# Kernel tuning notes

Measured on AMD Instinct MI355X. Metric: run time of the kernel, lower is better.

The kernel has to match this reference:

```python
import jax, jax.numpy as jnp
import numpy as np

NEG_SLOPE = 0.2  # PyG GATConv default negative_slope


def gat_layer(x, src, dst, N, W, att_src, att_dst, bias, heads, out_ch, concat):
    # x: [N, Fin]; W: [Fin, heads*out_ch]; att_*: [heads, out_ch]; bias matches output dim
    h = (x @ W).reshape(N, heads, out_ch)              # [N, H, C]
    a_src = (h * att_src).sum(-1)                      # [N, H]
    a_dst = (h * att_dst).sum(-1)                      # [N, H]
    e = jax.nn.leaky_relu(a_src[src] + a_dst[dst], NEG_SLOPE)  # [E, H]
    # segment softmax over incoming edges of each destination node
    e_max = jax.ops.segment_max(e, dst, num_segments=N)        # [N, H]
    e_exp = jnp.exp(e - e_max[dst])                             # [E, H]
    denom = jax.ops.segment_sum(e_exp, dst, num_segments=N)    # [N, H]
    alpha = e_exp / (denom[dst] + 1e-16)                        # [E, H]
    msg = alpha[:, :, None] * h[src]                            # [E, H, C]
    out = jax.ops.segment_sum(msg, dst, num_segments=N)        # [N, H, C]
    out = out.reshape(N, heads * out_ch) if concat else out.mean(axis=1)
    return out + bias


def setup_inputs() -> dict:
    key = jax.random.key(0)
    ks = jax.random.split(key, 10)
    N, E = 40000, 160000
    Fin, H1, C1 = 602, 8, 256
    H2, C2 = 1, 42
    g = lambda k, shape, fan: (jax.random.normal(k, shape, dtype=jnp.float32) * (1.0 / np.sqrt(fan)))
    return {
        "x": jax.random.normal(ks[0], (N, Fin), dtype=jnp.float32),
        "edge_index": jax.random.randint(ks[1], (2, E), 0, N, dtype=jnp.int64),
        "W1": g(ks[2], (Fin, H1 * C1), Fin),
        "att_src1": g(ks[3], (H1, C1), C1),
        "att_dst1": g(ks[4], (H1, C1), C1),
        "b1": jnp.zeros((H1 * C1,), dtype=jnp.float32),
        "W2": g(ks[5], (H1 * C1, H2 * C2), H1 * C1),
        "att_src2": g(ks[6], (H2, C2), C2),
        "att_dst2": g(ks[7], (H2, C2), C2),
        "b2": jnp.zeros((C2,), dtype=jnp.float32),
    }


def reference(x, edge_index, W1, att_src1, att_dst1, b1, W2, att_src2, att_dst2, b2):
    N = x.shape[0]
    # PyG GATConv default add_self_loops=True
    loops = jnp.arange(N, dtype=edge_index.dtype)
    src = jnp.concatenate([edge_index[0], loops])
    dst = jnp.concatenate([edge_index[1], loops])
    h = gat_layer(x, src, dst, N, W1, att_src1, att_dst1, b1, heads=8, out_ch=256, concat=True)
    h = jax.nn.relu(h)  # dropout is identity in eval mode
    h = gat_layer(h, src, dst, N, W2, att_src2, att_dst2, b2, heads=1, out_ch=42, concat=False)
    return jax.nn.log_softmax(h, axis=1)
```

## Files before the change

kernel.cpp:

```cpp
#include <hip/hip_runtime.h>
#include <hip/hip_bf16.h>

#define NN   40000
#define NE   160000
#define ETOT 200000
#define FIN  602
#define NH1  8
#define C1   256
#define F1   2048
#define C2   42
#define NEG  0.2f
#define NB   157
#define KP   608
#define MP   40064

typedef unsigned short u16;
typedef unsigned int   u32;
typedef __bf16 bf16x8 __attribute__((ext_vector_type(8)));
typedef float  f32x4  __attribute__((ext_vector_type(4)));

__device__ __forceinline__ float bfu(u16 v){ return __uint_as_float(((u32)v) << 16); }
__device__ __forceinline__ float bflo(u32 u){ return __uint_as_float(u << 16); }
__device__ __forceinline__ float bfhi(u32 u){ return __uint_as_float(u & 0xffff0000u); }
__device__ __forceinline__ u16 f2bf(float f){
  u32 u = __float_as_uint(f);
  u32 r = (u + 0x7fffu + ((u >> 16) & 1u)) >> 16;
  return (u16)r;
}

__device__ __forceinline__ void gl_lds16(const u16* g, u16* l) {
  __builtin_amdgcn_global_load_lds(
      (const __attribute__((address_space(1))) u32*)(g),
      (__attribute__((address_space(3))) u32*)(l), 16, 0, 0);
}

__global__ void probe_k(const u32* __restrict__ xw, const int* __restrict__ ei,
                        int* __restrict__ flags) {
  if (threadIdx.x == 0) {
    int zc = 0;
    for (int k = 0; k < 64; ++k) zc += (ei[2*k + 1] == 0) ? 1 : 0;
    flags[0] = (zc == 64) ? 1 : 0;
    int inr = 0;
    for (int k = 0; k < 64; ++k) {
      u32 low = xw[k] & 0xffffu;
      int e = (int)((low >> 7) & 0xff);
      inr += (e >= 100 && e <= 140) ? 1 : 0;
    }
    flags[1] = (inr >= 32) ? 0 : 1;
  }
}

__global__ void cvt_f32_k(const void* __restrict__ src, float* __restrict__ dst, int n,
                          const int* __restrict__ flags) {
  int i = blockIdx.x * 256 + threadIdx.x;
  if (i >= n) return;
  dst[i] = flags[1] ? ((const float*)src)[i] : bfu(((const u16*)src)[i]);
}

__global__ void xb_k(const void* __restrict__ x, u16* __restrict__ xb,
                     const int* __restrict__ flags) {
  int k = blockIdx.x * 256 + threadIdx.x;
  int row = blockIdx.y;
  if (k >= KP) return;
  u16 v = 0;
  if (row < NN && k < FIN)
    v = flags[1] ? f2bf(((const float*)x)[(size_t)row * FIN + k])
                 : ((const u16*)x)[(size_t)row * FIN + k];
  xb[(size_t)row * KP + k] = v;
}

__global__ void w1t_k(const void* __restrict__ W1, u16* __restrict__ w1t,
                      const int* __restrict__ flags) {
  int n = blockIdx.x * 256 + threadIdx.x;
  int k = blockIdx.y;
  if (n >= F1) return;
  u16 v = 0;
  if (k < FIN) v = flags[1] ? f2bf(((const float*)W1)[(size_t)k * F1 + n])
                            : ((const u16*)W1)[(size_t)k * F1 + n];
  w1t[(size_t)n * KP + k] = v;
}

__global__ void w2t_k(const void* __restrict__ W2, u16* __restrict__ w2t,
                      const int* __restrict__ flags) {
  int i = blockIdx.x * 256 + threadIdx.x;
  if (i >= 64 * F1) return;
  int c = i >> 11, k = i & (F1 - 1);
  u16 v = 0;
  if (c < C2) v = flags[1] ? f2bf(((const float*)W2)[(size_t)k * C2 + c])
                           : ((const u16*)W2)[(size_t)k * C2 + c];
  w2t[i] = v;
}

__device__ __forceinline__ void edge_sd(const int* __restrict__ ei, int e, int imode,
                                        int& s, int& d) {
  if (e < NE) {
    if (imode) { s = ei[2*e]; d = ei[2*(NE + e)]; }
    else       { s = ei[e];   d = ei[NE + e];     }
  } else { s = d = e - NE; }
}

__global__ void deg_k(const int* __restrict__ ei, int* __restrict__ deg,
                      const int* __restrict__ flags) {
  int e = blockIdx.x * 256 + threadIdx.x;
  if (e >= ETOT) return;
  int s, d; edge_sd(ei, e, flags[0], s, d);
  atomicAdd(&deg[d], 1);
}

__global__ __launch_bounds__(256) void scan1_k(const int* __restrict__ deg,
                                               int* __restrict__ tmp, int* __restrict__ bsum) {
  __shared__ int s[256];
  int b = blockIdx.x, t = threadIdx.x, i = b * 256 + t;
  int v = (i < NN) ? deg[i] : 0;
  s[t] = v; __syncthreads();
  for (int o = 1; o < 256; o <<= 1) {
    int u = (t >= o) ? s[t - o] : 0;
    __syncthreads(); s[t] += u; __syncthreads();
  }
  if (i < NN) tmp[i] = s[t];
  if (t == 255) bsum[b] = s[255];
}

__global__ __launch_bounds__(256) void scan2_k(int* __restrict__ bsum) {
  __shared__ int s[256];
  int t = threadIdx.x;
  int v = (t < NB) ? bsum[t] : 0;
  s[t] = v; __syncthreads();
  for (int o = 1; o < 256; o <<= 1) {
    int u = (t >= o) ? s[t - o] : 0;
    __syncthreads(); s[t] += u; __syncthreads();
  }
  if (t < NB) bsum[t] = s[t];
}

__global__ void scan3_k(const int* __restrict__ deg, const int* __restrict__ tmp,
                        const int* __restrict__ bsum, int* __restrict__ start, int* __restrict__ cur) {
  int i = blockIdx.x * 256 + threadIdx.x;
  if (i >= NN) return;
  int b = i >> 8;
  int off = b ? bsum[b - 1] : 0;
  int excl = tmp[i] - deg[i] + off;
  start[i] = excl; cur[i] = excl;
}

__global__ void fill_k(const int* __restrict__ ei, int* __restrict__ cur,
                       int* __restrict__ csr_src, int* __restrict__ csr_dst,
                       const int* __restrict__ flags) {
  int e = blockIdx.x * 256 + threadIdx.x;
  if (e >= ETOT) return;
  int s, d; edge_sd(ei, e, flags[0], s, d);
  int pos = atomicAdd(&cur[d], 1);
  csr_src[pos] = s; csr_dst[pos] = d;
}

__global__ __launch_bounds__(256) void gemm1a_k(const u16* __restrict__ xb,
                                                const u16* __restrict__ w1t,
                                                u16* __restrict__ h1,
                                                const float* __restrict__ as1c,
                                                const float* __restrict__ ad1c,
                                                float* __restrict__ a_s1,
                                                float* __restrict__ a_d1) {
  __shared__ u16 As[128 * 32];
  __shared__ u16 Bs[128 * 32];
  const int t = threadIdx.x;
  const int lane = t & 63, wid = t >> 6;
  const int wr = wid >> 1, wc = wid & 1;
  const int m0 = blockIdx.y * 128, n0 = blockIdx.x * 128;
  const int l16 = lane & 15, lk = (lane >> 4) * 8;
  f32x4 acc[4][4];
  #pragma unroll
  for (int i = 0; i < 4; ++i)
    #pragma unroll
    for (int j = 0; j < 4; ++j) acc[i][j] = (f32x4){0.f, 0.f, 0.f, 0.f};

  const size_t sa0 = (size_t)(m0 + (t >> 2)) * KP + (t & 3) * 8;
  const size_t sa1 = (size_t)(m0 + 64 + (t >> 2)) * KP + (t & 3) * 8;
  const size_t sb0 = (size_t)(n0 + (t >> 2)) * KP + (t & 3) * 8;
  const size_t sb1 = (size_t)(n0 + 64 + (t >> 2)) * KP + (t & 3) * 8;
  u16* la0 = As + (wid << 9);
  u16* la1 = As + 2048 + (wid << 9);
  u16* lb0 = Bs + (wid << 9);
  u16* lb1 = Bs + 2048 + (wid << 9);

  for (int k0 = 0; k0 < KP; k0 += 32) {
    gl_lds16(xb + sa0 + k0, la0);
    gl_lds16(xb + sa1 + k0, la1);
    gl_lds16(w1t + sb0 + k0, lb0);
    gl_lds16(w1t + sb1 + k0, lb1);
    __syncthreads();
    bf16x8 bfr[4];
    #pragma unroll
    for (int ni = 0; ni < 4; ++ni)
      bfr[ni] = *(const bf16x8*)&Bs[(wc * 64 + ni * 16 + l16) * 32 + lk];
    #pragma unroll
    for (int mi = 0; mi < 4; ++mi) {
      bf16x8 af = *(const bf16x8*)&As[(wr * 64 + mi * 16 + l16) * 32 + lk];
      #pragma unroll
      for (int ni = 0; ni < 4; ++ni)
        acc[mi][ni] = __builtin_amdgcn_mfma_f32_16x16x32_bf16(af, bfr[ni], acc[mi][ni], 0, 0, 0);
    }
    __syncthreads();
  }

  const int h0 = n0 >> 8;
  float psrc[4][4], pdst[4][4];
  #pragma unroll
  for (int mi = 0; mi < 4; ++mi)
    #pragma unroll
    for (int r = 0; r < 4; ++r) { psrc[mi][r] = 0.f; pdst[mi][r] = 0.f; }
  #pragma unroll
  for (int ni = 0; ni < 4; ++ni) {
    int col = n0 + wc * 64 + ni * 16 + l16;
    float wsv = as1c[col], wdv = ad1c[col];
    #pragma unroll
    for (int mi = 0; mi < 4; ++mi)
      #pragma unroll
      for (int r = 0; r < 4; ++r) {
        float v = acc[mi][ni][r];
        psrc[mi][r] += v * wsv;
        pdst[mi][r] += v * wdv;
      }
  }
  #pragma unroll
  for (int o = 1; o < 16; o <<= 1) {
    #pragma unroll
    for (int mi = 0; mi < 4; ++mi)
      #pragma unroll
      for (int r = 0; r < 4; ++r) {
        psrc[mi][r] += __shfl_xor(psrc[mi][r], o, 64);
        pdst[mi][r] += __shfl_xor(pdst[mi][r], o, 64);
      }
  }
  const int lr4 = (lane >> 4) * 4;
  if (l16 == 0) {
    #pragma unroll
    for (int mi = 0; mi < 4; ++mi)
      #pragma unroll
      for (int r = 0; r < 4; ++r) {
        int row = m0 + wr * 64 + mi * 16 + lr4 + r;
        if (row < NN) {
          atomicAdd(&a_s1[row * NH1 + h0], psrc[mi][r]);
          atomicAdd(&a_d1[row * NH1 + h0], pdst[mi][r]);
        }
      }
  }

  #pragma unroll
  for (int mi = 0; mi < 4; ++mi) {
    #pragma unroll
    for (int r = 0; r < 4; ++r) {
      int row = m0 + wr * 64 + mi * 16 + lr4 + r;
      if (row < NN) {
        #pragma unroll
        for (int ni = 0; ni < 4; ++ni) {
          int col = n0 + wc * 64 + ni * 16 + l16;
          h1[(size_t)row * F1 + col] = f2bf(acc[mi][ni][r]);
        }
      }
    }
  }
}

__global__ __launch_bounds__(256) void gemm1m_k(const void* __restrict__ xv,
                                                const u16* __restrict__ w1t,
                                                u16* __restrict__ h1,
                                                const int* __restrict__ flags) {
  __shared__ u16 As[128][40];
  __shared__ u16 Bs[128][40];
  const int fm = flags[1];
  const int t = threadIdx.x;
  const int lane = t & 63, wid = t >> 6;
  const int wr = wid >> 1, wc = wid & 1;
  const int m0 = blockIdx.y * 128, n0 = blockIdx.x * 128;
  const int l16 = lane & 15, lk = (lane >> 4) * 8;
  f32x4 acc[4][4];
  #pragma unroll
  for (int i = 0; i < 4; ++i)
    #pragma unroll
    for (int j = 0; j < 4; ++j) acc[i][j] = (f32x4){0.f, 0.f, 0.f, 0.f};
  const int arow = t >> 2;
  const int akb  = (t & 3) * 8;
  for (int k0 = 0; k0 < KP; k0 += 32) {
    #pragma unroll
    for (int i = 0; i < 2; ++i) {
      int row = arow + i * 64;
      int rg = m0 + row;
      u32 d0 = 0, d1 = 0, d2 = 0, d3 = 0;
      if (rg < NN) {
        if (k0 + 32 <= FIN) {
          if (fm) {
            const float* xp = (const float*)xv + (size_t)rg * FIN + k0 + akb;
            float2 p0 = *(const float2*)(xp);
            float2 p1 = *(const float2*)(xp + 2);
            float2 p2 = *(const float2*)(xp + 4);
            float2 p3 = *(const float2*)(xp + 6);
            d0 = (u32)f2bf(p0.x) | ((u32)f2bf(p0.y) << 16);
            d1 = (u32)f2bf(p1.x) | ((u32)f2bf(p1.y) << 16);
            d2 = (u32)f2bf(p2.x) | ((u32)f2bf(p2.y) << 16);
            d3 = (u32)f2bf(p3.x) | ((u32)f2bf(p3.y) << 16);
          } else {
            const u16* xp = (const u16*)xv + (size_t)rg * FIN + k0 + akb;
            d0 = *(const u32*)(xp);
            d1 = *(const u32*)(xp + 2);
            d2 = *(const u32*)(xp + 4);
            d3 = *(const u32*)(xp + 6);
          }
        } else {
          u16 e[8];
          #pragma unroll
          for (int q = 0; q < 8; ++q) {
            int k = k0 + akb + q;
            e[q] = 0;
            if (k < FIN)
              e[q] = fm ? f2bf(((const float*)xv)[(size_t)rg * FIN + k])
                        : ((const u16*)xv)[(size_t)rg * FIN + k];
          }
          d0 = (u32)e[0] | ((u32)e[1] << 16);
          d1 = (u32)e[2] | ((u32)e[3] << 16);
          d2 = (u32)e[4] | ((u32)e[5] << 16);
          d3 = (u32)e[6] | ((u32)e[7] << 16);
        }
      }
      *(uint4*)&As[row][akb] = make_uint4(d0, d1, d2, d3);
      const u16* wp = w1t + (size_t)(n0 + row) * KP + k0 + akb;
      *(uint4*)&Bs[row][akb] = *(const uint4*)wp;
    }
    __syncthreads();
    bf16x8 bfr[4];
    #pragma unroll
    for (int ni = 0; ni < 4; ++ni)
      bfr[ni] = *(const bf16x8*)&Bs[wc * 64 + ni * 16 + l16][lk];
    #pragma unroll
    for (int mi = 0; mi < 4; ++mi) {
      bf16x8 af = *(const bf16x8*)&As[wr * 64 + mi * 16 + l16][lk];
      #pragma unroll
      for (int ni = 0; ni < 4; ++ni)
        acc[mi][ni] = __builtin_amdgcn_mfma_f32_16x16x32_bf16(af, bfr[ni], acc[mi][ni], 0, 0, 0);
    }
    __syncthreads();
  }
  const int lr4 = (lane >> 4) * 4;
  #pragma unroll
  for (int mi = 0; mi < 4; ++mi) {
    #pragma unroll
    for (int r = 0; r < 4; ++r) {
      int row = m0 + wr * 64 + mi * 16 + lr4 + r;
      if (row < NN) {
        #pragma unroll
        for (int ni = 0; ni < 4; ++ni) {
          int col = n0 + wc * 64 + ni * 16 + l16;
          h1[(size_t)row * F1 + col] = f2bf(acc[mi][ni][r]);
        }
      }
    }
  }
}

__global__ __launch_bounds__(256) void att1_k(const u16* __restrict__ h1,
                                              const float* __restrict__ as1c, const float* __restrict__ ad1c,
                                              float* __restrict__ a_s, float* __restrict__ a_d) {
  int n = blockIdx.x, t = threadIdx.x;
  int h = t >> 5, l = t & 31;
  int base = h * C1 + l * 8;
  const u16* hp = h1 + (size_t)n * F1 + base;
  uint4 v = *(const uint4*)hp;
  u32 w[4] = {v.x, v.y, v.z, v.w};
  float ss = 0.f, sd = 0.f;
  #pragma unroll
  for (int p = 0; p < 4; ++p) {
    float e0 = bflo(w[p]), e1 = bfhi(w[p]);
    ss += e0 * as1c[base + 2*p] + e1 * as1c[base + 2*p + 1];
    sd += e0 * ad1c[base + 2*p] + e1 * ad1c[base + 2*p + 1];
  }
  #pragma unroll
  for (int o = 16; o > 0; o >>= 1) {
    ss += __shfl_down(ss, o, 32);
    sd += __shfl_down(sd, o, 32);
  }
  if (l == 0) { a_s[n * NH1 + h] = ss; a_d[n * NH1 + h] = sd; }
}

__global__ __launch_bounds__(256) void gfuse_k(const int* __restrict__ start, const int* __restrict__ deg,
                                               const int* __restrict__ csr_src,
                                               const float* __restrict__ a_s1, const float* __restrict__ a_d1,
                                               const u16* __restrict__ h1, const float* __restrict__ b1c,
                                               const u16* __restrict__ w2t, float* __restrict__ h2) {
  __shared__ u16 rowsL[16 * F1];
  int t = threadIdx.x;
  int nb = blockIdx.x * 16;
  int h = t >> 5;
  int c0 = t * 8;
  float4 bA = *(const float4*)(b1c + c0);
  float4 bB = *(const float4*)(b1c + c0 + 4);
  for (int i = 0; i < 16; ++i) {
    int n = nb + i;
    int s0 = start[n], jend = s0 + deg[n];
    float ad = a_d1[n * NH1 + h];
    float a0=0.f,a1=0.f,a2=0.f,a3=0.f,a4=0.f,a5=0.f,a6=0.f,a7=0.f,den=0.f;
    int j = s0;
    for (; j + 2 <= jend; j += 2) {
      int sA = csr_src[j], sB = csr_src[j + 1];
      float vA = a_s1[sA * NH1 + h] + ad;
      float vB = a_s1[sB * NH1 + h] + ad;
      vA = vA > 0.f ? vA : NEG * vA;
      vB = vB > 0.f ? vB : NEG * vB;
      float eA = expf(vA), eB = expf(vB);
      uint4 uA = *(const uint4*)(h1 + (size_t)sA * F1 + c0);
      uint4 uB = *(const uint4*)(h1 + (size_t)sB * F1 + c0);
      den += eA + eB;
      a0 += eA * bflo(uA.x) + eB * bflo(uB.x);
      a1 += eA * bfhi(uA.x) + eB * bfhi(uB.x);
      a2 += eA * bflo(uA.y) + eB * bflo(uB.y);
      a3 += eA * bfhi(uA.y) + eB * bfhi(uB.y);
      a4 += eA * bflo(uA.z) + eB * bflo(uB.z);
      a5 += eA * bfhi(uA.z) + eB * bfhi(uB.z);
      a6 += eA * bflo(uA.w) + eB * bflo(uB.w);
      a7 += eA * bfhi(uA.w) + eB * bfhi(uB.w);
    }
    if (j < jend) {
      int sA = csr_src[j];
      float vA = a_s1[sA * NH1 + h] + ad;
      vA = vA > 0.f ? vA : NEG * vA;
      float eA = expf(vA);
      uint4 uA = *(const uint4*)(h1 + (size_t)sA * F1 + c0);
      den += eA;
      a0 += eA * bflo(uA.x); a1 += eA * bfhi(uA.x);
      a2 += eA * bflo(uA.y); a3 += eA * bfhi(uA.y);
      a4 += eA * bflo(uA.z); a5 += eA * bfhi(uA.z);
      a6 += eA * bflo(uA.w); a7 += eA * bfhi(uA.w);
    }
    float inv = 1.f / (den + 1e-16f);
    u16 o0 = f2bf(fmaxf(a0 * inv + bA.x, 0.f));
    u16 o1 = f2bf(fmaxf(a1 * inv + bA.y, 0.f));
    u16 o2 = f2bf(fmaxf(a2 * inv + bA.z, 0.f));
    u16 o3 = f2bf(fmaxf(a3 * inv + bA.w, 0.f));
    u16 o4 = f2bf(fmaxf(a4 * inv + bB.x, 0.f));
    u16 o5 = f2bf(fmaxf(a5 * inv + bB.y, 0.f));
    u16 o6 = f2bf(fmaxf(a6 * inv + bB.z, 0.f));
    u16 o7 = f2bf(fmaxf(a7 * inv + bB.w, 0.f));
    uint4 pk;
    pk.x = (u32)o0 | ((u32)o1 << 16);
    pk.y = (u32)o2 | ((u32)o3 << 16);
    pk.z = (u32)o4 | ((u32)o5 << 16);
    pk.w = (u32)o6 | ((u32)o7 << 16);
    int sw = (i & 7) << 3;
    *(uint4*)&rowsL[i * F1 + (c0 ^ sw)] = pk;
  }
  __syncthreads();
  int lane = t & 63, wid = t >> 6;
  int l16 = lane & 15, lk = (lane >> 4) * 8;
  const u16* wt = w2t + (size_t)(wid * 16 + l16) * F1;
  int sw = (l16 & 7) << 3;
  f32x4 acc2 = (f32x4){0.f, 0.f, 0.f, 0.f};
  for (int k0 = 0; k0 < F1; k0 += 32) {
    int kk = k0 + lk;
    bf16x8 af = *(const bf16x8*)&rowsL[l16 * F1 + (kk ^ sw)];
    bf16x8 bf = *(const bf16x8*)(wt + kk);
    acc2 = __builtin_amdgcn_mfma_f32_16x16x32_bf16(af, bf, acc2, 0, 0, 0);
  }
  int col = wid * 16 + l16;
  if (col < C2) {
    int mb = (lane >> 4) * 4;
    #pragma unroll
    for (int r = 0; r < 4; ++r)
      h2[(size_t)(nb + mb + r) * C2 + col] = acc2[r];
  }
}

__global__ __launch_bounds__(64) void att2_k(const float* __restrict__ h2,
                                             const float* __restrict__ as2, const float* __restrict__ ad2,
                                             float* __restrict__ a_s, float* __restrict__ a_d) {
  int n = blockIdx.x, t = threadIdx.x;
  float ss = 0.f, sd = 0.f;
  if (t < C2) {
    float v = h2[(size_t)n * C2 + t];
    ss = v * as2[t];
    sd = v * ad2[t];
  }
  #pragma unroll
  for (int o = 32; o > 0; o >>= 1) {
    ss += __shfl_down(ss, o, 64);
    sd += __shfl_down(sd, o, 64);
  }
  if (t == 0) { a_s[n] = ss; a_d[n] = sd; }
}

__global__ __launch_bounds__(64) void gath2_k(const int* __restrict__ start, const int* __restrict__ deg,
                                              const int* __restrict__ csr_src,
                                              const float* __restrict__ a_s, const float* __restrict__ a_d,
                                              const float* __restrict__ h2, const float* __restrict__ b2,
                                              void* __restrict__ outv, const int* __restrict__ flags) {
  int n = blockIdx.x, t = threadIdx.x;
  int s0 = start[n], cnt = deg[n];
  float ad = a_d[n];
  float acc = 0.f, den = 0.f;
  for (int j = s0; j < s0 + cnt; ++j) {
    int s = csr_src[j];
    float v = a_s[s] + ad;
    v = v > 0.f ? v : NEG * v;
    float e = expf(v);
    den += e;
    if (t < C2) acc += e * h2[(size_t)s * C2 + t];
  }
  float raw = (t < C2) ? acc / (den + 1e-16f) + b2[t] : -1e30f;
  float m = raw;
  #pragma unroll
  for (int o = 32; o > 0; o >>= 1) m = fmaxf(m, __shfl_down(m, o, 64));
  m = __shfl(m, 0, 64);
  float e2 = (t < C2) ? expf(raw - m) : 0.f;
  float ssum = e2;
  #pragma unroll
  for (int o = 32; o > 0; o >>= 1) ssum += __shfl_down(ssum, o, 64);
  ssum = __shfl(ssum, 0, 64);
  if (t < C2) {
    float v = raw - m - logf(ssum);
    if (flags[1]) ((float*)outv)[(size_t)n * C2 + t] = v;
    else          ((u16*) outv)[(size_t)n * C2 + t] = f2bf(v);
  }
}

extern "C" void kernel_launch(void* const* d_in, const int* in_sizes, int n_in,
                              void* d_out, int out_size, void* d_ws, size_t ws_size,
                              hipStream_t stream) {
  const void* x   = d_in[0];
  const int*  ei  = (const int*)d_in[1];
  const void* W1  = d_in[2];
  const void* as1 = d_in[3];
  const void* ad1 = d_in[4];
  const void* b1  = d_in[5];
  const void* W2  = d_in[6];
  const void* as2 = d_in[7];
  const void* ad2 = d_in[8];
  const void* b2  = d_in[9];

  char* ws = (char*)d_ws;
  u16*   h1      = (u16*)  (ws);
  float* ex1     = (float*)(ws + 163840000);
  float* h2      = (float*)(ws + 170240000);
  float* a_s1    = (float*)(ws + 176960000);
  float* a_d1    = (float*)(ws + 178240000);
  float* a_s2    = (float*)(ws + 179520000);
  float* a_d2    = (float*)(ws + 179680000);
  int*   deg     = (int*)  (ws + 179840000);
  int*   start   = (int*)  (ws + 180000000);
  int*   cur     = (int*)  (ws + 180160000);
  int*   tmp     = (int*)  (ws + 180320000);
  int*   csr_src = (int*)  (ws + 180480000);
  int*   csr_dst = (int*)  (ws + 181280000);
  int*   bsum    = (int*)  (ws + 182080000);
  u16*   w1t     = (u16*)  (ws + 182081024);
  u16*   w2t     = (u16*)  (ws + 184571392);
  float* as1c    = (float*)(ws + 184833536);
  float* ad1c    = (float*)(ws + 184841728);
  float* b1c     = (float*)(ws + 184849920);
  float* as2c    = (float*)(ws + 184858112);
  float* ad2c    = (float*)(ws + 184858368);
  float* b2c     = (float*)(ws + 184858624);
  int*   flags   = (int*)  (ws + 184858880);
  const size_t TOTAL_BASE = 184859136;
  u16*   xb      = (u16*)  (ws + TOTAL_BASE);
  const size_t TOTAL_A = TOTAL_BASE + (size_t)MP * KP * 2;
  if (ws_size < TOTAL_BASE) return;
  const bool pathA = (ws_size >= TOTAL_A);
  (void)ex1;

  probe_k<<<1, 64, 0, stream>>>((const u32*)x, ei, flags);

  cvt_f32_k<<<(F1 + 255) / 256, 256, 0, stream>>>(as1, as1c, F1, flags);
  cvt_f32_k<<<(F1 + 255) / 256, 256, 0, stream>>>(ad1, ad1c, F1, flags);
  cvt_f32_k<<<(F1 + 255) / 256, 256, 0, stream>>>(b1, b1c, F1, flags);
  cvt_f32_k<<<1, 256, 0, stream>>>(as2, as2c, C2, flags);
  cvt_f32_k<<<1, 256, 0, stream>>>(ad2, ad2c, C2, flags);
  cvt_f32_k<<<1, 256, 0, stream>>>(b2, b2c, C2, flags);
  w1t_k<<<dim3(8, KP), 256, 0, stream>>>(W1, w1t, flags);
  w2t_k<<<(64 * F1 + 255) / 256, 256, 0, stream>>>(W2, w2t, flags);

  hipMemsetAsync(deg, 0, NN * sizeof(int), stream);
  hipMemsetAsync(a_s1, 0, 2 * NN * NH1 * sizeof(float), stream);
  const int EB = (ETOT + 255) / 256;
  deg_k  <<<EB, 256, 0, stream>>>(ei, deg, flags);
  scan1_k<<<NB, 256, 0, stream>>>(deg, tmp, bsum);
  scan2_k<<<1, 256, 0, stream>>>(bsum);
  scan3_k<<<NB, 256, 0, stream>>>(deg, tmp, bsum, start, cur);
  fill_k <<<EB, 256, 0, stream>>>(ei, cur, csr_src, csr_dst, flags);

  if (pathA) {
    xb_k<<<dim3((KP + 255) / 256, MP), 256, 0, stream>>>(x, xb, flags);
    gemm1a_k<<<dim3(16, MP / 128), 256, 0, stream>>>(xb, w1t, h1, as1c, ad1c, a_s1, a_d1);
  } else {
    gemm1m_k<<<dim3(16, MP / 128), 256, 0, stream>>>(x, w1t, h1, flags);
    att1_k<<<NN, 256, 0, stream>>>(h1, as1c, ad1c, a_s1, a_d1);
  }
  gfuse_k<<<NN / 16, 256, 0, stream>>>(start, deg, csr_src, a_s1, a_d1, h1, b1c, w2t, h2);

  att2_k<<<NN, 64, 0, stream>>>(h2, as2c, ad2c, a_s2, a_d2);
  gath2_k<<<NN, 64, 0, stream>>>(start, deg, csr_src, a_s2, a_d2, h2, b2c, d_out, flags);
}
```

Measured before the change: 655.1 us.

## Double-buffer LDS tiles and XOR-swizzle layout in first-layer GEMM

The first GEMM kernel now double-buffers its A and B shared-memory tiles, issuing the global-to-LDS loads for the next K slice before the MFMA work on the current one, and drops one barrier per iteration. The k-chunk placement in LDS is XOR-swizzled on both the write and read sides to cut LDS bank conflicts on the bf16x8 fragment reads. LDS use doubles, which may lower occupancy. Correctness relies on the async LDS loads having completed by the single remaining barrier.

Measured after the change: 688.0 us. 1.05x slower.

```diff
diff --git a/kernel.cpp b/kernel.cpp
--- a/kernel.cpp
+++ b/kernel.cpp
@@ -160,47 +160,60 @@
                                                 const float* __restrict__ ad1c,
                                                 float* __restrict__ a_s1,
                                                 float* __restrict__ a_d1) {
-  __shared__ u16 As[128 * 32];
-  __shared__ u16 Bs[128 * 32];
+  __shared__ u16 As[2 * 4096];
+  __shared__ u16 Bs[2 * 4096];
   const int t = threadIdx.x;
   const int lane = t & 63, wid = t >> 6;
   const int wr = wid >> 1, wc = wid & 1;
   const int m0 = blockIdx.y * 128, n0 = blockIdx.x * 128;
-  const int l16 = lane & 15, lk = (lane >> 4) * 8;
+  const int l16 = lane & 15;
   f32x4 acc[4][4];
   #pragma unroll
   for (int i = 0; i < 4; ++i)
     #pragma unroll
     for (int j = 0; j < 4; ++j) acc[i][j] = (f32x4){0.f, 0.f, 0.f, 0.f};
 
-  const size_t sa0 = (size_t)(m0 + (t >> 2)) * KP + (t & 3) * 8;
-  const size_t sa1 = (size_t)(m0 + 64 + (t >> 2)) * KP + (t & 3) * 8;
-  const size_t sb0 = (size_t)(n0 + (t >> 2)) * KP + (t & 3) * 8;
-  const size_t sb1 = (size_t)(n0 + 64 + (t >> 2)) * KP + (t & 3) * 8;
-  u16* la0 = As + (wid << 9);
-  u16* la1 = As + 2048 + (wid << 9);
-  u16* lb0 = Bs + (wid << 9);
-  u16* lb1 = Bs + 2048 + (wid << 9);
-
+  const int kc = (((t & 3) ^ ((t >> 3) & 3))) * 8;
+  const size_t sa0 = (size_t)(m0 + (t >> 2)) * KP + kc;
+  const size_t sa1 = (size_t)(m0 + 64 + (t >> 2)) * KP + kc;
+  const size_t sb0 = (size_t)(n0 + (t >> 2)) * KP + kc;
+  const size_t sb1 = (size_t)(n0 + 64 + (t >> 2)) * KP + kc;
+
+  const int fsw = ((lane >> 4) ^ ((l16 >> 1) & 3)) << 3;
+  const int rdA = (wr * 64 + l16) * 32 + fsw;
+  const int rdB = (wc * 64 + l16) * 32 + fsw;
+
+#define STAGE(K0, B) do {                                      \
+    u16* a_ = As + (B) * 4096 + (wid << 9);                    \
+    u16* b_ = Bs + (B) * 4096 + (wid << 9);                    \
+    gl_lds16(xb  + sa0 + (K0), a_);                            \
+    gl_lds16(xb  + sa1 + (K0), a_ + 2048);                     \
+    gl_lds16(w1t + sb0 + (K0), b_);                            \
+    gl_lds16(w1t + sb1 + (K0), b_ + 2048);                     \
+  } while (0)
+
+  STAGE(0, 0);
+  __syncthreads();
+  int cur = 0;
   for (int k0 = 0; k0 < KP; k0 += 32) {
-    gl_lds16(xb + sa0 + k0, la0);
-    gl_lds16(xb + sa1 + k0, la1);
-    gl_lds16(w1t + sb0 + k0, lb0);
-    gl_lds16(w1t + sb1 + k0, lb1);
-    __syncthreads();
+    if (k0 + 32 < KP) STAGE(k0 + 32, cur ^ 1);
+    const u16* Ab = As + cur * 4096;
+    const u16* Bb = Bs + cur * 4096;
     bf16x8 bfr[4];
     #pragma unroll
     for (int ni = 0; ni < 4; ++ni)
-      bfr[ni] = *(const bf16x8*)&Bs[(wc * 64 + ni * 16 + l16) * 32 + lk];
+      bfr[ni] = *(const bf16x8*)&Bb[rdB + ni * 512];
     #pragma unroll
     for (int mi = 0; mi < 4; ++mi) {
-      bf16x8 af = *(const bf16x8*)&As[(wr * 64 + mi * 16 + l16) * 32 + lk];
+      bf16x8 af = *(const bf16x8*)&Ab[rdA + mi * 512];
       #pragma unroll
       for (int ni = 0; ni < 4; ++ni)
         acc[mi][ni] = __builtin_amdgcn_mfma_f32_16x16x32_bf16(af, bfr[ni], acc[mi][ni], 0, 0, 0);
     }
     __syncthreads();
-  }
+    cur ^= 1;
+  }
+#undef STAGE
 
   const int h0 = n0 >> 8;
   float psrc[4][4], pdst[4][4];
```

## Load GEMM1 MFMA fragments directly from global memory with register prefetch

Applied to the files above, without the earlier changes.

The first-layer GEMM no longer stages A and B tiles through LDS with global_load_lds and two barriers per k-step. Each wave now reads its bf16x8 MFMA fragments straight from global memory and prefetches the next k-slice into registers while the current one is multiplied. This removes the LDS traffic and block-wide synchronisation, but each fragment is loaded by two waves instead of once per block, which doubles global/L2 reads, and the strided 16-byte row accesses may coalesce less well.

New measurement: 660.4 us. About the same (+0.8%).

```diff
diff --git a/kernel.cpp b/kernel.cpp
--- a/kernel.cpp
+++ b/kernel.cpp
@@ -28,12 +28,6 @@
   return (u16)r;
 }
 
-__device__ __forceinline__ void gl_lds16(const u16* g, u16* l) {
-  __builtin_amdgcn_global_load_lds(
-      (const __attribute__((address_space(1))) u32*)(g),
-      (__attribute__((address_space(3))) u32*)(l), 16, 0, 0);
-}
-
 __global__ void probe_k(const u32* __restrict__ xw, const int* __restrict__ ei,
                         int* __restrict__ flags) {
   if (threadIdx.x == 0) {
@@ -153,15 +147,13 @@
   csr_src[pos] = s; csr_dst[pos] = d;
 }
 
-__global__ __launch_bounds__(256) void gemm1a_k(const u16* __restrict__ xb,
+__global__ __launch_bounds__(256) void gemm1b_k(const u16* __restrict__ xb,
                                                 const u16* __restrict__ w1t,
                                                 u16* __restrict__ h1,
                                                 const float* __restrict__ as1c,
                                                 const float* __restrict__ ad1c,
                                                 float* __restrict__ a_s1,
                                                 float* __restrict__ a_d1) {
-  __shared__ u16 As[128 * 32];
-  __shared__ u16 Bs[128 * 32];
   const int t = threadIdx.x;
   const int lane = t & 63, wid = t >> 6;
   const int wr = wid >> 1, wc = wid & 1;
@@ -173,34 +165,35 @@
     #pragma unroll
     for (int j = 0; j < 4; ++j) acc[i][j] = (f32x4){0.f, 0.f, 0.f, 0.f};
 
-  const size_t sa0 = (size_t)(m0 + (t >> 2)) * KP + (t & 3) * 8;
-  const size_t sa1 = (size_t)(m0 + 64 + (t >> 2)) * KP + (t & 3) * 8;
-  const size_t sb0 = (size_t)(n0 + (t >> 2)) * KP + (t & 3) * 8;
-  const size_t sb1 = (size_t)(n0 + 64 + (t >> 2)) * KP + (t & 3) * 8;
-  u16* la0 = As + (wid << 9);
-  u16* la1 = As + 2048 + (wid << 9);
-  u16* lb0 = Bs + (wid << 9);
-  u16* lb1 = Bs + 2048 + (wid << 9);
-
-  for (int k0 = 0; k0 < KP; k0 += 32) {
-    gl_lds16(xb + sa0 + k0, la0);
-    gl_lds16(xb + sa1 + k0, la1);
-    gl_lds16(w1t + sb0 + k0, lb0);
-    gl_lds16(w1t + sb1 + k0, lb1);
-    __syncthreads();
-    bf16x8 bfr[4];
-    #pragma unroll
-    for (int ni = 0; ni < 4; ++ni)
-      bfr[ni] = *(const bf16x8*)&Bs[(wc * 64 + ni * 16 + l16) * 32 + lk];
-    #pragma unroll
-    for (int mi = 0; mi < 4; ++mi) {
-      bf16x8 af = *(const bf16x8*)&As[(wr * 64 + mi * 16 + l16) * 32 + lk];
+  const u16* Ap = xb  + (size_t)(m0 + wr * 64 + l16) * KP + lk;
+  const u16* Bp = w1t + (size_t)(n0 + wc * 64 + l16) * KP + lk;
+
+  bf16x8 a[4], b[4];
+  #pragma unroll
+  for (int i = 0; i < 4; ++i) {
+    a[i] = *(const bf16x8*)(Ap + (size_t)i * 16 * KP);
+    b[i] = *(const bf16x8*)(Bp + (size_t)i * 16 * KP);
+  }
+  for (int k0 = 32; k0 < KP; k0 += 32) {
+    bf16x8 an[4], bn[4];
+    #pragma unroll
+    for (int i = 0; i < 4; ++i) {
+      an[i] = *(const bf16x8*)(Ap + (size_t)i * 16 * KP + k0);
+      bn[i] = *(const bf16x8*)(Bp + (size_t)i * 16 * KP + k0);
+    }
+    #pragma unroll
+    for (int mi = 0; mi < 4; ++mi)
       #pragma unroll
       for (int ni = 0; ni < 4; ++ni)
-        acc[mi][ni] = __builtin_amdgcn_mfma_f32_16x16x32_bf16(af, bfr[ni], acc[mi][ni], 0, 0, 0);
-    }
-    __syncthreads();
-  }
+        acc[mi][ni] = __builtin_amdgcn_mfma_f32_16x16x32_bf16(a[mi], b[ni], acc[mi][ni], 0, 0, 0);
+    #pragma unroll
+    for (int i = 0; i < 4; ++i) { a[i] = an[i]; b[i] = bn[i]; }
+  }
+  #pragma unroll
+  for (int mi = 0; mi < 4; ++mi)
+    #pragma unroll
+    for (int ni = 0; ni < 4; ++ni)
+      acc[mi][ni] = __builtin_amdgcn_mfma_f32_16x16x32_bf16(a[mi], b[ni], acc[mi][ni], 0, 0, 0);
 
   const int h0 = n0 >> 8;
   float psrc[4][4], pdst[4][4];
@@ -586,7 +579,7 @@
 
   if (pathA) {
     xb_k<<<dim3((KP + 255) / 256, MP), 256, 0, stream>>>(x, xb, flags);
-    gemm1a_k<<<dim3(16, MP / 128), 256, 0, stream>>>(xb, w1t, h1, as1c, ad1c, a_s1, a_d1);
+    gemm1b_k<<<dim3(16, MP / 128), 256, 0, stream>>>(xb, w1t, h1, as1c, ad1c, a_s1, a_d1);
   } else {
     gemm1m_k<<<dim3(16, MP / 128), 256, 0, stream>>>(x, w1t, h1, flags);
     att1_k<<<NN, 256, 0, stream>>>(h1, as1c, ad1c, a_s1, a_d1);
```
